# Optimization experiments

Measured on AMD Instinct MI355X. Metric: run time of the kernel, lower is better.

Reference implementation:

```python
import jax, jax.numpy as jnp
import numpy as np

H = 16        # num_heads
NB = 64       # n_buckets
NH = 6        # n_hyperplanes = log2(NB)


def setup_inputs() -> dict:
    key = jax.random.key(0)
    k = jax.random.split(key, 6)
    E = 1024
    B, S = 2, 2048
    return {
        "x": jax.random.normal(k[0], (B, S, E), jnp.float32),
        "Wq": jax.random.normal(k[1], (E, E), jnp.float32) * (E ** -0.5),
        "bq": jax.random.normal(k[2], (E,), jnp.float32) * 0.02,
        "Wv": jax.random.normal(k[3], (E, E), jnp.float32) * (E ** -0.5),
        "bv": jax.random.normal(k[4], (E,), jnp.float32) * 0.02,
        "hyperplanes": jax.random.normal(k[5], (E // H + 1, NH), jnp.float32),
    }


def reference(x, Wq, bq, Wv, bv, hyperplanes):
    B, S, E = x.shape
    Dh = E // H
    # projections (torch Linear: x @ W.T + b)
    q = (x @ Wq.T + bq).reshape(B, S, H, Dh)
    v = (x @ Wv.T + bv).reshape(B, S, H, Dh)

    # LSH buckets from q: append a ones column, sign-project onto hyperplanes
    qa = jnp.concatenate([q, jnp.ones((B, S, H, 1), q.dtype)], axis=-1)  # [B,S,H,Dh+1]
    proj = jnp.einsum('bshe,en->bshn', qa, hyperplanes)
    bits = (proj >= 0).astype(jnp.int32)
    buckets = jnp.einsum('bshn,n->bsh', bits, 2 ** jnp.arange(NH, dtype=jnp.int32))  # [B,S,H]
    b_hs = buckets.transpose(0, 2, 1)  # [B,H,S]

    q = q.transpose(0, 2, 1, 3)  # [B,H,S,Dh]
    v = v.transpose(0, 2, 1, 3)

    # The original sums, over all NB buckets i, of (q with bucket-i tokens zeroed)
    # times its transpose. Closed form of that sum:
    #   sum_i (1-d[bs,i])(1-d[bt,i]) = NB - 2 + [bs == bt]
    scores = jnp.einsum('bhsd,bhtd->bhst', q, q) / jnp.sqrt(jnp.float32(E))
    same = (b_hs[:, :, :, None] == b_hs[:, :, None, :]).astype(scores.dtype)
    coeff = (NB - 2) + same
    attn = jax.nn.softmax(scores * coeff, axis=-1)  # [B,H,S,S]

    out = jnp.einsum('bhst,bhtd->bhsd', attn, v)
    return out.transpose(0, 2, 1, 3).reshape(B, S, E)
```

## Files before the change

### kernel.cpp

```cpp
#include <hip/hip_runtime.h>


typedef short short8 __attribute__((ext_vector_type(8)));
typedef float f32x4 __attribute__((ext_vector_type(4)));
typedef unsigned short us4 __attribute__((ext_vector_type(4)));

__device__ __forceinline__ float bff(unsigned short h) {
    return __uint_as_float(((unsigned int)h) << 16);
}
__device__ __forceinline__ unsigned short f2bf(float f) {
    unsigned int u = __float_as_uint(f);
    u += 0x7fffu + ((u >> 16) & 1u);
    return (unsigned short)(u >> 16);
}

__device__ __forceinline__ void glds16(const unsigned short* g, unsigned short* l) {
    __builtin_amdgcn_global_load_lds(
        (const __attribute__((address_space(1))) unsigned int*)g,
        (__attribute__((address_space(3))) unsigned int*)l, 16, 0, 0);
}

__global__ __launch_bounds__(256) void split_all(
    const float* __restrict__ x, const float* __restrict__ Wq,
    const float* __restrict__ Wv,
    unsigned short* __restrict__ xh, unsigned short* __restrict__ xl,
    unsigned short* __restrict__ Wqh, unsigned short* __restrict__ Wql,
    unsigned short* __restrict__ Wvh)
{
    const int blk = blockIdx.x;
    const float* in;
    unsigned short *hi, *lo;
    int idx;
    if (blk < 4096) {
        idx = blk * 256 + threadIdx.x; in = x; hi = xh; lo = xl;
    } else if (blk < 5120) {
        idx = (blk - 4096) * 256 + threadIdx.x; in = Wq; hi = Wqh; lo = Wql;
    } else {
        idx = (blk - 5120) * 256 + threadIdx.x; in = Wv; hi = Wvh; lo = nullptr;
    }
    const float4 v = ((const float4*)in)[idx];
    us4 h;
    h.x = f2bf(v.x); h.y = f2bf(v.y); h.z = f2bf(v.z); h.w = f2bf(v.w);
    ((us4*)hi)[idx] = h;
    if (lo) {
        us4 l;
        l.x = f2bf(v.x - bff(h.x)); l.y = f2bf(v.y - bff(h.y));
        l.z = f2bf(v.z - bff(h.z)); l.w = f2bf(v.w - bff(h.w));
        ((us4*)lo)[idx] = l;
    }
}

__global__ __launch_bounds__(256, 1) void gemm_qv(
    const unsigned short* __restrict__ xh, const unsigned short* __restrict__ xl,
    const unsigned short* __restrict__ wqh, const unsigned short* __restrict__ wql,
    const unsigned short* __restrict__ wvh,
    const float* __restrict__ bq, const float* __restrict__ bv,
    float* __restrict__ Qf, unsigned short* __restrict__ Qb,
    unsigned short* __restrict__ Qlo, unsigned short* __restrict__ Vt)
{
    __shared__ unsigned short Ah[128 * 64], Al[128 * 64];
    __shared__ unsigned short Bh[128 * 64], Bl[128 * 64];

    const int tid = threadIdx.x;
    const int w = tid >> 6, lane = tid & 63;
    const int i = lane & 15, qd = lane >> 4;
    const int l8 = lane >> 3, j = lane & 7;
    const int nw = w * 32;
    const int blk = blockIdx.x;
    const bool isq = blk < 256;

    f32x4 acc[8][2];
#pragma unroll
    for (int a = 0; a < 8; ++a)
#pragma unroll
        for (int b2 = 0; b2 < 2; ++b2) acc[a][b2] = f32x4{0.f, 0.f, 0.f, 0.f};

    const int gro = ((j ^ l8) << 3);

    if (isq) {
        const int m0 = (blk >> 3) * 128;
        const int n0 = (blk & 7) * 128;
        for (int k0 = 0; k0 < 1024; k0 += 64) {
            __syncthreads();
#pragma unroll
            for (int c = 0; c < 4; ++c) {
                const int r = w * 32 + c * 8;
                const size_t gx = (size_t)(m0 + r + l8) * 1024 + k0 + gro;
                const size_t gw = (size_t)(n0 + r + l8) * 1024 + k0 + gro;
                glds16(xh + gx, &Ah[r * 64]);
                glds16(xl + gx, &Al[r * 64]);
                glds16(wqh + gw, &Bh[r * 64]);
                glds16(wql + gw, &Bl[r * 64]);
            }
            __syncthreads();
#pragma unroll
            for (int kc = 0; kc < 2; ++kc) {
                const int ch = (((kc * 4 + qd) ^ (i & 7)) << 3);
                short8 ah[8], al[8], bh2[2], bl2[2];
#pragma unroll
                for (int mm = 0; mm < 8; ++mm) {
                    ah[mm] = *(const short8*)&Ah[(mm * 16 + i) * 64 + ch];
                    al[mm] = *(const short8*)&Al[(mm * 16 + i) * 64 + ch];
                }
#pragma unroll
                for (int nn = 0; nn < 2; ++nn) {
                    bh2[nn] = *(const short8*)&Bh[(nw + nn * 16 + i) * 64 + ch];
                    bl2[nn] = *(const short8*)&Bl[(nw + nn * 16 + i) * 64 + ch];
                }
#pragma unroll
                for (int mm = 0; mm < 8; ++mm)
#pragma unroll
                    for (int nn = 0; nn < 2; ++nn) {
                        acc[mm][nn] = __builtin_amdgcn_mfma_f32_16x16x32_bf16(
                            ah[mm], bh2[nn], acc[mm][nn], 0, 0, 0);
                        acc[mm][nn] = __builtin_amdgcn_mfma_f32_16x16x32_bf16(
                            al[mm], bh2[nn], acc[mm][nn], 0, 0, 0);
                        acc[mm][nn] = __builtin_amdgcn_mfma_f32_16x16x32_bf16(
                            ah[mm], bl2[nn], acc[mm][nn], 0, 0, 0);
                    }
            }
        }
#pragma unroll
        for (int mm = 0; mm < 8; ++mm)
#pragma unroll
            for (int nn = 0; nn < 2; ++nn)
#pragma unroll
                for (int rr = 0; rr < 4; ++rr) {
                    const int row = m0 + mm * 16 + qd * 4 + rr;
                    const int col = n0 + nw + nn * 16 + i;
                    const float v = acc[mm][nn][rr] + bq[col];
                    Qf[(size_t)row * 1024 + col] = v;
                    const unsigned short hs = f2bf(v);
                    const float lo = v - bff(hs);
                    const int b = row >> 11, s = row & 2047;
                    const int hh = col >> 6, d = col & 63;
                    const size_t oi = ((size_t)((b << 4) + hh) * 2048 + s) * 64 + d;
                    Qb[oi] = hs;
                    Qlo[oi] = f2bf(lo);
                }
    } else {
        const int b2 = blk - 256;
        const int m0 = (b2 & 7) * 128;
        const int n0 = (b2 >> 3) * 128;
        for (int k0 = 0; k0 < 1024; k0 += 64) {
            __syncthreads();
#pragma unroll
            for (int c = 0; c < 4; ++c) {
                const int r = w * 32 + c * 8;
                glds16(wvh + (size_t)(m0 + r + l8) * 1024 + k0 + gro, &Ah[r * 64]);
                glds16(xh + (size_t)(n0 + r + l8) * 1024 + k0 + gro, &Bh[r * 64]);
            }
            __syncthreads();
#pragma unroll
            for (int kc = 0; kc < 2; ++kc) {
                const int ch = (((kc * 4 + qd) ^ (i & 7)) << 3);
                short8 af[8], bf2[2];
#pragma unroll
                for (int mm = 0; mm < 8; ++mm)
                    af[mm] = *(const short8*)&Ah[(mm * 16 + i) * 64 + ch];
#pragma unroll
                for (int nn = 0; nn < 2; ++nn)
                    bf2[nn] = *(const short8*)&Bh[(nw + nn * 16 + i) * 64 + ch];
#pragma unroll
                for (int mm = 0; mm < 8; ++mm)
#pragma unroll
                    for (int nn = 0; nn < 2; ++nn)
                        acc[mm][nn] = __builtin_amdgcn_mfma_f32_16x16x32_bf16(
                            af[mm], bf2[nn], acc[mm][nn], 0, 0, 0);
            }
        }
#pragma unroll
        for (int mm = 0; mm < 8; ++mm)
#pragma unroll
            for (int nn = 0; nn < 2; ++nn)
#pragma unroll
                for (int rr = 0; rr < 4; ++rr) {
                    const int rch = m0 + mm * 16 + qd * 4 + rr;
                    const int tok = n0 + nw + nn * 16 + i;
                    const float v = acc[mm][nn][rr] + bv[rch];
                    const int b = tok >> 11, s = tok & 2047;
                    Vt[((size_t)(b * 1024 + rch)) * 2048 + s] = f2bf(v);
                }
    }
}

__global__ __launch_bounds__(256) void bucket_kernel(
    const float* __restrict__ Qf, const float* __restrict__ hp,
    int* __restrict__ buckets, float* __restrict__ rown)
{
    __shared__ float hpl[65 * 6];
    const int tid = threadIdx.x;
    if (tid < 65 * 6) hpl[tid] = hp[tid];
    __syncthreads();

    const int idx = blockIdx.x * 256 + tid;
    const int m = idx >> 4, h = idx & 15;
    const float4* q4 = (const float4*)(Qf + (size_t)m * 1024 + h * 64);

    float pj[6];
    float nrm = 0.f;
#pragma unroll
    for (int n = 0; n < 6; ++n) pj[n] = hpl[64 * 6 + n];
    for (int d4 = 0; d4 < 16; ++d4) {
        const float4 qv = q4[d4];
        nrm = fmaf(qv.x, qv.x, nrm); nrm = fmaf(qv.y, qv.y, nrm);
        nrm = fmaf(qv.z, qv.z, nrm); nrm = fmaf(qv.w, qv.w, nrm);
#pragma unroll
        for (int n = 0; n < 6; ++n) {
            pj[n] = fmaf(qv.x, hpl[(d4 * 4 + 0) * 6 + n], pj[n]);
            pj[n] = fmaf(qv.y, hpl[(d4 * 4 + 1) * 6 + n], pj[n]);
            pj[n] = fmaf(qv.z, hpl[(d4 * 4 + 2) * 6 + n], pj[n]);
            pj[n] = fmaf(qv.w, hpl[(d4 * 4 + 3) * 6 + n], pj[n]);
        }
    }
    int bkt = 0;
#pragma unroll
    for (int n = 0; n < 6; ++n) bkt |= (pj[n] >= 0.f) << n;
    const int off = ((m >> 11) * 16 + h) * 2048 + (m & 2047);
    buckets[off] = bkt;
    rown[off] = nrm;
}

__global__ __launch_bounds__(256, 2) void attn_kernel(
    const unsigned short* __restrict__ Qb, const unsigned short* __restrict__ Qlo,
    const unsigned short* __restrict__ Vt, const int* __restrict__ bks,
    const float* __restrict__ rown, float* __restrict__ out)
{
    __shared__ unsigned short Khi[2][64 * 64];
    __shared__ unsigned short Klo[2][64 * 64];
    __shared__ unsigned short Vs[2][64 * 64];
    __shared__ unsigned short P[4][16 * 64];
    __shared__ float smax[4];

    const int tid = threadIdx.x;
    const int w = tid >> 6, lane = tid & 63;
    const int i = lane & 15, qd = lane >> 4;
    const int l8 = lane >> 3, j = lane & 7;
    const int bh = blockIdx.x;
    const int qbase = blockIdx.y * 128 + w * 32;

    const unsigned short* Qh = Qb + (size_t)bh * 2048 * 64;
    const unsigned short* Ql = Qlo + (size_t)bh * 2048 * 64;
    const unsigned short* Vb = Vt + (size_t)bh * 64 * 2048;
    const int* bk = bks + bh * 2048;
    const float* rnh = rown + bh * 2048;
    unsigned short* Pw = &P[w][0];

    float lm = 0.f;
    for (int t = tid; t < 2048; t += 256) lm = fmaxf(lm, rnh[t]);
#pragma unroll
    for (int msk = 1; msk < 64; msk <<= 1) lm = fmaxf(lm, __shfl_xor(lm, msk));
    if (lane == 0) smax[w] = lm;
    __syncthreads();
    const float sqM = sqrtf(fmaxf(fmaxf(smax[0], smax[1]),
                                  fmaxf(smax[2], smax[3])));

    float m2row[2][4], lrun[2][4];
    int qbr[2][4];
#pragma unroll
    for (int ms = 0; ms < 2; ++ms)
#pragma unroll
        for (int r = 0; r < 4; ++r) {
            const int row = qbase + ms * 16 + qd * 4 + r;
            m2row[ms][r] = 2.84030586f * sqrtf(rnh[row]) * sqM + 0.72134754f;
            qbr[ms][r] = bk[row];
            lrun[ms][r] = 0.f;
        }

    short8 aqh0[2], aqh1[2], aql0[2], aql1[2];
#pragma unroll
    for (int ms = 0; ms < 2; ++ms) {
        const unsigned short* qp = Qh + (size_t)(qbase + ms * 16 + i) * 64 + qd * 8;
        const unsigned short* lp = Ql + (size_t)(qbase + ms * 16 + i) * 64 + qd * 8;
        aqh0[ms] = *(const short8*)qp; aqh1[ms] = *(const short8*)(qp + 32);
        aql0[ms] = *(const short8*)lp; aql1[ms] = *(const short8*)(lp + 32);
    }

    f32x4 o[2][4];
#pragma unroll
    for (int ms = 0; ms < 2; ++ms)
#pragma unroll
        for (int d = 0; d < 4; ++d) o[ms][d] = f32x4{0.f, 0.f, 0.f, 0.f};

    const int swz = ((j ^ l8) << 3);

    for (int t0 = 0; t0 < 2048; t0 += 128) {
        __syncthreads();
#pragma unroll
        for (int hf = 0; hf < 2; ++hf) {
            const int t0h = t0 + hf * 64;
#pragma unroll
            for (int c2 = 0; c2 < 2; ++c2) {
                const int r = w * 16 + c2 * 8 + l8;
                glds16(Qh + (size_t)(t0h + r) * 64 + swz, &Khi[hf][w * 1024 + c2 * 512]);
                glds16(Ql + (size_t)(t0h + r) * 64 + swz, &Klo[hf][w * 1024 + c2 * 512]);
                glds16(Vb + (size_t)r * 2048 + t0h + swz, &Vs[hf][w * 1024 + c2 * 512]);
            }
        }
        __syncthreads();

#pragma unroll
        for (int hf = 0; hf < 2; ++hf) {
            const int t0h = t0 + hf * 64;

            f32x4 s[2][4];
            int kb[4];
#pragma unroll
            for (int sub = 0; sub < 4; ++sub) {
                const int kr = sub * 16 + i;
                const int sw = i & 7;
                const short8 bh0 = *(const short8*)&Khi[hf][kr * 64 + ((qd ^ sw) << 3)];
                const short8 bh1 = *(const short8*)&Khi[hf][kr * 64 + (((qd + 4) ^ sw) << 3)];
                const short8 bl0 = *(const short8*)&Klo[hf][kr * 64 + ((qd ^ sw) << 3)];
                const short8 bl1 = *(const short8*)&Klo[hf][kr * 64 + (((qd + 4) ^ sw) << 3)];
                kb[sub] = bk[t0h + kr];
#pragma unroll
                for (int ms = 0; ms < 2; ++ms) {
                    f32x4 t = f32x4{0.f, 0.f, 0.f, 0.f};
                    t = __builtin_amdgcn_mfma_f32_16x16x32_bf16(aqh0[ms], bh0, t, 0, 0, 0);
                    t = __builtin_amdgcn_mfma_f32_16x16x32_bf16(aqh1[ms], bh1, t, 0, 0, 0);
                    t = __builtin_amdgcn_mfma_f32_16x16x32_bf16(aql0[ms], bh0, t, 0, 0, 0);
                    t = __builtin_amdgcn_mfma_f32_16x16x32_bf16(aql1[ms], bh1, t, 0, 0, 0);
                    t = __builtin_amdgcn_mfma_f32_16x16x32_bf16(aqh0[ms], bl0, t, 0, 0, 0);
                    t = __builtin_amdgcn_mfma_f32_16x16x32_bf16(aqh1[ms], bl1, t, 0, 0, 0);
                    s[ms][sub] = t;
                }
            }

            short8 vb0[4], vb1[4];
#pragma unroll
            for (int dsub = 0; dsub < 4; ++dsub) {
                const int dr = dsub * 16 + i;
                const int sw = i & 7;
                vb0[dsub] = *(const short8*)&Vs[hf][dr * 64 + ((qd ^ sw) << 3)];
                vb1[dsub] = *(const short8*)&Vs[hf][dr * 64 + (((qd + 4) ^ sw) << 3)];
            }

#pragma unroll
            for (int ms = 0; ms < 2; ++ms) {
#pragma unroll
                for (int sub = 0; sub < 4; ++sub)
#pragma unroll
                    for (int r = 0; r < 4; ++r) {
                        const float c2f = (kb[sub] == qbr[ms][r]) ? 2.84030586f
                                                                  : 2.79522164f;
                        const float p = exp2f(fmaf(s[ms][sub][r], c2f, -m2row[ms][r]));
                        lrun[ms][r] += p;
                        const unsigned int pu = __float_as_uint(p);
                        const int row = qd * 4 + r, col = sub * 16 + i;
                        Pw[row * 64 + (((col >> 3) ^ (row & 7)) << 3) + (col & 7)] =
                            (unsigned short)(pu >> 16);
                    }
                const short8 pa0 = *(const short8*)&Pw[i * 64 + ((qd ^ (i & 7)) << 3)];
                const short8 pa1 = *(const short8*)&Pw[i * 64 + (((qd + 4) ^ (i & 7)) << 3)];
#pragma unroll
                for (int dsub = 0; dsub < 4; ++dsub) {
                    o[ms][dsub] = __builtin_amdgcn_mfma_f32_16x16x32_bf16(
                        pa0, vb0[dsub], o[ms][dsub], 0, 0, 0);
                    o[ms][dsub] = __builtin_amdgcn_mfma_f32_16x16x32_bf16(
                        pa1, vb1[dsub], o[ms][dsub], 0, 0, 0);
                }
            }
        }
    }

#pragma unroll
    for (int ms = 0; ms < 2; ++ms)
#pragma unroll
        for (int r = 0; r < 4; ++r) {
#pragma unroll
            for (int msk = 1; msk < 16; msk <<= 1)
                lrun[ms][r] += __shfl_xor(lrun[ms][r], msk);
        }
    const int b = bh >> 4, h = bh & 15;
#pragma unroll
    for (int ms = 0; ms < 2; ++ms)
#pragma unroll
        for (int dsub = 0; dsub < 4; ++dsub)
#pragma unroll
            for (int r = 0; r < 4; ++r) {
                const float v = o[ms][dsub][r] / lrun[ms][r];
                const int srow = qbase + ms * 16 + qd * 4 + r;
                out[((size_t)(b * 2048 + srow)) * 1024 + h * 64 + dsub * 16 + i] = v;
            }
}

extern "C" void kernel_launch(void* const* d_in, const int* in_sizes, int n_in,
                              void* d_out, int out_size, void* d_ws, size_t ws_size,
                              hipStream_t stream)
{
    const float* x  = (const float*)d_in[0];
    const float* Wq = (const float*)d_in[1];
    const float* bq = (const float*)d_in[2];
    const float* Wv = (const float*)d_in[3];
    const float* bv = (const float*)d_in[4];
    const float* hp = (const float*)d_in[5];
    float* out = (float*)d_out;

    char* ws = (char*)d_ws;
    const size_t MB = (size_t)1 << 20;
    unsigned short* xh  = (unsigned short*)(ws);
    unsigned short* xl  = (unsigned short*)(ws + 8 * MB);
    unsigned short* Wqh = (unsigned short*)(ws + 16 * MB);
    unsigned short* Wql = (unsigned short*)(ws + 18 * MB);
    unsigned short* Wvh = (unsigned short*)(ws + 20 * MB);
    unsigned short* Qb  = (unsigned short*)(ws + 22 * MB);
    unsigned short* Qlo = (unsigned short*)(ws + 30 * MB);
    unsigned short* Vt  = (unsigned short*)(ws + 38 * MB);
    float*          Qf  = (float*)(ws + 46 * MB);
    int*        buckets = (int*)(ws + 62 * MB);
    float*         rown = (float*)(ws + 62 * MB + 256 * 1024);

    split_all<<<dim3(6144), 256, 0, stream>>>(x, Wq, Wv, xh, xl, Wqh, Wql, Wvh);
    gemm_qv<<<dim3(512), 256, 0, stream>>>(xh, xl, Wqh, Wql, Wvh, bq, bv,
                                           Qf, Qb, Qlo, Vt);
    bucket_kernel<<<dim3(256), 256, 0, stream>>>(Qf, hp, buckets, rown);
    attn_kernel<<<dim3(32, 16), 256, 0, stream>>>(Qb, Qlo, Vt, buckets, rown, out);
}
```

Baseline: 221.7 us.

## Drop fp32 Q buffer, raise GEMM occupancy, shrink attention tile to 64

The Q/V GEMM no longer writes an fp32 copy of Q. The bucket kernel instead rebuilds Q from the bf16 hi/lo pair, which is already stored in head-major layout. The GEMM asks for two blocks per SM and loads A fragments inside the mm loop, cutting register pressure. The attention kernel drops from a 128-key step of two 64-key halves to a single 64-key tile, halving LDS use at the cost of twice as many barriers; bucket projections now use the hi+lo reconstruction and may differ slightly from fp32.

```diff
diff --git a/kernel.cpp b/kernel.cpp
--- a/kernel.cpp
+++ b/kernel.cpp
@@ -50,13 +50,13 @@
     }
 }
 
-__global__ __launch_bounds__(256, 1) void gemm_qv(
+__global__ __launch_bounds__(256, 2) void gemm_qv(
     const unsigned short* __restrict__ xh, const unsigned short* __restrict__ xl,
     const unsigned short* __restrict__ wqh, const unsigned short* __restrict__ wql,
     const unsigned short* __restrict__ wvh,
     const float* __restrict__ bq, const float* __restrict__ bv,
-    float* __restrict__ Qf, unsigned short* __restrict__ Qb,
-    unsigned short* __restrict__ Qlo, unsigned short* __restrict__ Vt)
+    unsigned short* __restrict__ Qb, unsigned short* __restrict__ Qlo,
+    unsigned short* __restrict__ Vt)
 {
     __shared__ unsigned short Ah[128 * 64], Al[128 * 64];
     __shared__ unsigned short Bh[128 * 64], Bl[128 * 64];
@@ -96,28 +96,26 @@
 #pragma unroll
             for (int kc = 0; kc < 2; ++kc) {
                 const int ch = (((kc * 4 + qd) ^ (i & 7)) << 3);
-                short8 ah[8], al[8], bh2[2], bl2[2];
-#pragma unroll
-                for (int mm = 0; mm < 8; ++mm) {
-                    ah[mm] = *(const short8*)&Ah[(mm * 16 + i) * 64 + ch];
-                    al[mm] = *(const short8*)&Al[(mm * 16 + i) * 64 + ch];
-                }
+                short8 bh2[2], bl2[2];
 #pragma unroll
                 for (int nn = 0; nn < 2; ++nn) {
                     bh2[nn] = *(const short8*)&Bh[(nw + nn * 16 + i) * 64 + ch];
                     bl2[nn] = *(const short8*)&Bl[(nw + nn * 16 + i) * 64 + ch];
                 }
 #pragma unroll
-                for (int mm = 0; mm < 8; ++mm)
+                for (int mm = 0; mm < 8; ++mm) {
+                    const short8 ah = *(const short8*)&Ah[(mm * 16 + i) * 64 + ch];
+                    const short8 al = *(const short8*)&Al[(mm * 16 + i) * 64 + ch];
 #pragma unroll
                     for (int nn = 0; nn < 2; ++nn) {
                         acc[mm][nn] = __builtin_amdgcn_mfma_f32_16x16x32_bf16(
-                            ah[mm], bh2[nn], acc[mm][nn], 0, 0, 0);
+                            ah, bh2[nn], acc[mm][nn], 0, 0, 0);
                         acc[mm][nn] = __builtin_amdgcn_mfma_f32_16x16x32_bf16(
-                            al[mm], bh2[nn], acc[mm][nn], 0, 0, 0);
+                            al, bh2[nn], acc[mm][nn], 0, 0, 0);
                         acc[mm][nn] = __builtin_amdgcn_mfma_f32_16x16x32_bf16(
-                            ah[mm], bl2[nn], acc[mm][nn], 0, 0, 0);
+                            ah, bl2[nn], acc[mm][nn], 0, 0, 0);
                     }
+                }
             }
         }
 #pragma unroll
@@ -129,7 +127,6 @@
                     const int row = m0 + mm * 16 + qd * 4 + rr;
                     const int col = n0 + nw + nn * 16 + i;
                     const float v = acc[mm][nn][rr] + bq[col];
-                    Qf[(size_t)row * 1024 + col] = v;
                     const unsigned short hs = f2bf(v);
                     const float lo = v - bff(hs);
                     const int b = row >> 11, s = row & 2047;
@@ -154,19 +151,18 @@
 #pragma unroll
             for (int kc = 0; kc < 2; ++kc) {
                 const int ch = (((kc * 4 + qd) ^ (i & 7)) << 3);
-                short8 af[8], bf2[2];
-#pragma unroll
-                for (int mm = 0; mm < 8; ++mm)
-                    af[mm] = *(const short8*)&Ah[(mm * 16 + i) * 64 + ch];
+                short8 bf2[2];
 #pragma unroll
                 for (int nn = 0; nn < 2; ++nn)
                     bf2[nn] = *(const short8*)&Bh[(nw + nn * 16 + i) * 64 + ch];
 #pragma unroll
-                for (int mm = 0; mm < 8; ++mm)
+                for (int mm = 0; mm < 8; ++mm) {
+                    const short8 af = *(const short8*)&Ah[(mm * 16 + i) * 64 + ch];
 #pragma unroll
                     for (int nn = 0; nn < 2; ++nn)
                         acc[mm][nn] = __builtin_amdgcn_mfma_f32_16x16x32_bf16(
-                            af[mm], bf2[nn], acc[mm][nn], 0, 0, 0);
+                            af, bf2[nn], acc[mm][nn], 0, 0, 0);
+                }
             }
         }
 #pragma unroll
@@ -185,7 +181,8 @@
 }
 
 __global__ __launch_bounds__(256) void bucket_kernel(
-    const float* __restrict__ Qf, const float* __restrict__ hp,
+    const unsigned short* __restrict__ Qb, const unsigned short* __restrict__ Qlo,
+    const float* __restrict__ hp,
     int* __restrict__ buckets, float* __restrict__ rown)
 {
     __shared__ float hpl[65 * 6];
@@ -194,31 +191,30 @@
     __syncthreads();
 
     const int idx = blockIdx.x * 256 + tid;
-    const int m = idx >> 4, h = idx & 15;
-    const float4* q4 = (const float4*)(Qf + (size_t)m * 1024 + h * 64);
+    const unsigned short* qh = Qb + (size_t)idx * 64;
+    const unsigned short* ql = Qlo + (size_t)idx * 64;
 
     float pj[6];
     float nrm = 0.f;
 #pragma unroll
     for (int n = 0; n < 6; ++n) pj[n] = hpl[64 * 6 + n];
-    for (int d4 = 0; d4 < 16; ++d4) {
-        const float4 qv = q4[d4];
-        nrm = fmaf(qv.x, qv.x, nrm); nrm = fmaf(qv.y, qv.y, nrm);
-        nrm = fmaf(qv.z, qv.z, nrm); nrm = fmaf(qv.w, qv.w, nrm);
-#pragma unroll
-        for (int n = 0; n < 6; ++n) {
-            pj[n] = fmaf(qv.x, hpl[(d4 * 4 + 0) * 6 + n], pj[n]);
-            pj[n] = fmaf(qv.y, hpl[(d4 * 4 + 1) * 6 + n], pj[n]);
-            pj[n] = fmaf(qv.z, hpl[(d4 * 4 + 2) * 6 + n], pj[n]);
-            pj[n] = fmaf(qv.w, hpl[(d4 * 4 + 3) * 6 + n], pj[n]);
+    for (int d8 = 0; d8 < 8; ++d8) {
+        const short8 vh = *(const short8*)(qh + d8 * 8);
+        const short8 vl = *(const short8*)(ql + d8 * 8);
+#pragma unroll
+        for (int e = 0; e < 8; ++e) {
+            const float q = bff((unsigned short)vh[e]) + bff((unsigned short)vl[e]);
+            nrm = fmaf(q, q, nrm);
+#pragma unroll
+            for (int n = 0; n < 6; ++n)
+                pj[n] = fmaf(q, hpl[(d8 * 8 + e) * 6 + n], pj[n]);
         }
     }
     int bkt = 0;
 #pragma unroll
     for (int n = 0; n < 6; ++n) bkt |= (pj[n] >= 0.f) << n;
-    const int off = ((m >> 11) * 16 + h) * 2048 + (m & 2047);
-    buckets[off] = bkt;
-    rown[off] = nrm;
+    buckets[idx] = bkt;
+    rown[idx] = nrm;
 }
 
 __global__ __launch_bounds__(256, 2) void attn_kernel(
@@ -226,9 +222,9 @@
     const unsigned short* __restrict__ Vt, const int* __restrict__ bks,
     const float* __restrict__ rown, float* __restrict__ out)
 {
-    __shared__ unsigned short Khi[2][64 * 64];
-    __shared__ unsigned short Klo[2][64 * 64];
-    __shared__ unsigned short Vs[2][64 * 64];
+    __shared__ unsigned short Khi[64 * 64];
+    __shared__ unsigned short Klo[64 * 64];
+    __shared__ unsigned short Vs[64 * 64];
     __shared__ unsigned short P[4][16 * 64];
     __shared__ float smax[4];
 
@@ -282,84 +278,74 @@
 #pragma unroll
         for (int d = 0; d < 4; ++d) o[ms][d] = f32x4{0.f, 0.f, 0.f, 0.f};
 
-    const int swz = ((j ^ l8) << 3);
-
-    for (int t0 = 0; t0 < 2048; t0 += 128) {
+    for (int t0 = 0; t0 < 2048; t0 += 64) {
         __syncthreads();
 #pragma unroll
-        for (int hf = 0; hf < 2; ++hf) {
-            const int t0h = t0 + hf * 64;
-#pragma unroll
-            for (int c2 = 0; c2 < 2; ++c2) {
-                const int r = w * 16 + c2 * 8 + l8;
-                glds16(Qh + (size_t)(t0h + r) * 64 + swz, &Khi[hf][w * 1024 + c2 * 512]);
-                glds16(Ql + (size_t)(t0h + r) * 64 + swz, &Klo[hf][w * 1024 + c2 * 512]);
-                glds16(Vb + (size_t)r * 2048 + t0h + swz, &Vs[hf][w * 1024 + c2 * 512]);
-            }
+        for (int c2 = 0; c2 < 2; ++c2) {
+            const int r = w * 16 + c2 * 8 + l8;
+            const int swz = ((j ^ l8) << 3);
+            glds16(Qh + (size_t)(t0 + r) * 64 + swz, &Khi[w * 1024 + c2 * 512]);
+            glds16(Ql + (size_t)(t0 + r) * 64 + swz, &Klo[w * 1024 + c2 * 512]);
+            glds16(Vb + (size_t)r * 2048 + t0 + swz, &Vs[w * 1024 + c2 * 512]);
         }
         __syncthreads();
 
-#pragma unroll
-        for (int hf = 0; hf < 2; ++hf) {
-            const int t0h = t0 + hf * 64;
-
-            f32x4 s[2][4];
-            int kb[4];
-#pragma unroll
-            for (int sub = 0; sub < 4; ++sub) {
-                const int kr = sub * 16 + i;
-                const int sw = i & 7;
-                const short8 bh0 = *(const short8*)&Khi[hf][kr * 64 + ((qd ^ sw) << 3)];
-                const short8 bh1 = *(const short8*)&Khi[hf][kr * 64 + (((qd + 4) ^ sw) << 3)];
-                const short8 bl0 = *(const short8*)&Klo[hf][kr * 64 + ((qd ^ sw) << 3)];
-                const short8 bl1 = *(const short8*)&Klo[hf][kr * 64 + (((qd + 4) ^ sw) << 3)];
-                kb[sub] = bk[t0h + kr];
-#pragma unroll
-                for (int ms = 0; ms < 2; ++ms) {
-                    f32x4 t = f32x4{0.f, 0.f, 0.f, 0.f};
-                    t = __builtin_amdgcn_mfma_f32_16x16x32_bf16(aqh0[ms], bh0, t, 0, 0, 0);
-                    t = __builtin_amdgcn_mfma_f32_16x16x32_bf16(aqh1[ms], bh1, t, 0, 0, 0);
-                    t = __builtin_amdgcn_mfma_f32_16x16x32_bf16(aql0[ms], bh0, t, 0, 0, 0);
-                    t = __builtin_amdgcn_mfma_f32_16x16x32_bf16(aql1[ms], bh1, t, 0, 0, 0);
-                    t = __builtin_amdgcn_mfma_f32_16x16x32_bf16(aqh0[ms], bl0, t, 0, 0, 0);
-                    t = __builtin_amdgcn_mfma_f32_16x16x32_bf16(aqh1[ms], bl1, t, 0, 0, 0);
-                    s[ms][sub] = t;
-                }
-            }
-
-            short8 vb0[4], vb1[4];
+        f32x4 s[2][4];
+        int kb[4];
+#pragma unroll
+        for (int sub = 0; sub < 4; ++sub) {
+            const int kr = sub * 16 + i;
+            const int sw = i & 7;
+            const short8 bh0 = *(const short8*)&Khi[kr * 64 + ((qd ^ sw) << 3)];
+            const short8 bh1 = *(const short8*)&Khi[kr * 64 + (((qd + 4) ^ sw) << 3)];
+            const short8 bl0 = *(const short8*)&Klo[kr * 64 + ((qd ^ sw) << 3)];
+            const short8 bl1 = *(const short8*)&Klo[kr * 64 + (((qd + 4) ^ sw) << 3)];
+            kb[sub] = bk[t0 + kr];
+#pragma unroll
+            for (int ms = 0; ms < 2; ++ms) {
+                f32x4 t = f32x4{0.f, 0.f, 0.f, 0.f};
+                t = __builtin_amdgcn_mfma_f32_16x16x32_bf16(aqh0[ms], bh0, t, 0, 0, 0);
+                t = __builtin_amdgcn_mfma_f32_16x16x32_bf16(aqh1[ms], bh1, t, 0, 0, 0);
+                t = __builtin_amdgcn_mfma_f32_16x16x32_bf16(aql0[ms], bh0, t, 0, 0, 0);
+                t = __builtin_amdgcn_mfma_f32_16x16x32_bf16(aql1[ms], bh1, t, 0, 0, 0);
+                t = __builtin_amdgcn_mfma_f32_16x16x32_bf16(aqh0[ms], bl0, t, 0, 0, 0);
+                t = __builtin_amdgcn_mfma_f32_16x16x32_bf16(aqh1[ms], bl1, t, 0, 0, 0);
+                s[ms][sub] = t;
+            }
+        }
+
+        short8 vb0[4], vb1[4];
+#pragma unroll
+        for (int dsub = 0; dsub < 4; ++dsub) {
+            const int dr = dsub * 16 + i;
+            const int sw = i & 7;
+            vb0[dsub] = *(const short8*)&Vs[dr * 64 + ((qd ^ sw) << 3)];
+            vb1[dsub] = *(const short8*)&Vs[dr * 64 + (((qd + 4) ^ sw) << 3)];
+        }
+
+#pragma unroll
+        for (int ms = 0; ms < 2; ++ms) {
+#pragma unroll
+            for (int sub = 0; sub < 4; ++sub)
+#pragma unroll
+                for (int r = 0; r < 4; ++r) {
+                    const float c2f = (kb[sub] == qbr[ms][r]) ? 2.84030586f
+                                                              : 2.79522164f;
+                    const float p = exp2f(fmaf(s[ms][sub][r], c2f, -m2row[ms][r]));
+                    lrun[ms][r] += p;
+                    const unsigned int pu = __float_as_uint(p);
+                    const int row = qd * 4 + r, col = sub * 16 + i;
+                    Pw[row * 64 + (((col >> 3) ^ (row & 7)) << 3) + (col & 7)] =
+                        (unsigned short)(pu >> 16);
+                }
+            const short8 pa0 = *(const short8*)&Pw[i * 64 + ((qd ^ (i & 7)) << 3)];
+            const short8 pa1 = *(const short8*)&Pw[i * 64 + (((qd + 4) ^ (i & 7)) << 3)];
 #pragma unroll
             for (int dsub = 0; dsub < 4; ++dsub) {
-                const int dr = dsub * 16 + i;
-                const int sw = i & 7;
-                vb0[dsub] = *(const short8*)&Vs[hf][dr * 64 + ((qd ^ sw) << 3)];
-                vb1[dsub] = *(const short8*)&Vs[hf][dr * 64 + (((qd + 4) ^ sw) << 3)];
-            }
-
-#pragma unroll
-            for (int ms = 0; ms < 2; ++ms) {
-#pragma unroll
-                for (int sub = 0; sub < 4; ++sub)
-#pragma unroll
-                    for (int r = 0; r < 4; ++r) {
-                        const float c2f = (kb[sub] == qbr[ms][r]) ? 2.84030586f
-                                                                  : 2.79522164f;
-                        const float p = exp2f(fmaf(s[ms][sub][r], c2f, -m2row[ms][r]));
-                        lrun[ms][r] += p;
-                        const unsigned int pu = __float_as_uint(p);
-                        const int row = qd * 4 + r, col = sub * 16 + i;
-                        Pw[row * 64 + (((col >> 3) ^ (row & 7)) << 3) + (col & 7)] =
-                            (unsigned short)(pu >> 16);
-                    }
-                const short8 pa0 = *(const short8*)&Pw[i * 64 + ((qd ^ (i & 7)) << 3)];
-                const short8 pa1 = *(const short8*)&Pw[i * 64 + (((qd + 4) ^ (i & 7)) << 3)];
-#pragma unroll
-                for (int dsub = 0; dsub < 4; ++dsub) {
-                    o[ms][dsub] = __builtin_amdgcn_mfma_f32_16x16x32_bf16(
-                        pa0, vb0[dsub], o[ms][dsub], 0, 0, 0);
-                    o[ms][dsub] = __builtin_amdgcn_mfma_f32_16x16x32_bf16(
-                        pa1, vb1[dsub], o[ms][dsub], 0, 0, 0);
-                }
+                o[ms][dsub] = __builtin_amdgcn_mfma_f32_16x16x32_bf16(
+                    pa0, vb0[dsub], o[ms][dsub], 0, 0, 0);
+                o[ms][dsub] = __builtin_amdgcn_mfma_f32_16x16x32_bf16(
+                    pa1, vb1[dsub], o[ms][dsub], 0, 0, 0);
             }
         }
     }
@@ -407,13 +393,12 @@
     unsigned short* Qb  = (unsigned short*)(ws + 22 * MB);
     unsigned short* Qlo = (unsigned short*)(ws + 30 * MB);
     unsigned short* Vt  = (unsigned short*)(ws + 38 * MB);
-    float*          Qf  = (float*)(ws + 46 * MB);
     int*        buckets = (int*)(ws + 62 * MB);
     float*         rown = (float*)(ws + 62 * MB + 256 * 1024);
 
     split_all<<<dim3(6144), 256, 0, stream>>>(x, Wq, Wv, xh, xl, Wqh, Wql, Wvh);
     gemm_qv<<<dim3(512), 256, 0, stream>>>(xh, xl, Wqh, Wql, Wvh, bq, bv,
-                                           Qf, Qb, Qlo, Vt);
-    bucket_kernel<<<dim3(256), 256, 0, stream>>>(Qf, hp, buckets, rown);
+                                           Qb, Qlo, Vt);
+    bucket_kernel<<<dim3(256), 256, 0, stream>>>(Qb, Qlo, hp, buckets, rown);
     attn_kernel<<<dim3(32, 16), 256, 0, stream>>>(Qb, Qlo, Vt, buckets, rown, out);
 }
```

After: 216.8 us. 2.2% less time.
